# Optimization experiments

Measured on AMD Instinct MI355X. Metric: run time of the kernel, lower is better.

The kernel has to match this reference:

```python
import jax, jax.numpy as jnp
import numpy as np

N = 131072      # points (rays x samples chunk)
E = 8           # spatial sub-networks (centroids)
DIN = 90        # encoded pos+dir features fed to sub-NeRFs (xyz_real=True -> x[:, 3:])
H = 256         # sub-NeRF hidden width
DOUT = 4        # rgb + sigma
MARGIN = 2.0    # boundary_margin
EPS = 1e-8


def setup_inputs() -> dict:
    key = jax.random.key(0)
    k = jax.random.split(key, 5)
    x_xyz = jax.random.uniform(k[0], (N, 3), dtype=jnp.float32)          # routing coords in [0,1)^3
    x_feat = jax.random.normal(k[1], (N, DIN), dtype=jnp.float32)        # encoded features
    x = jnp.concatenate([x_xyz, x_feat], axis=1)                         # [N, 3+DIN]
    centroids = jax.random.uniform(k[2], (E, 3), dtype=jnp.float32)
    W1 = jax.random.normal(k[3], (E, DIN, H), dtype=jnp.float32) * 0.05
    b1 = jnp.zeros((E, H), dtype=jnp.float32)
    W2 = jax.random.normal(k[4], (E, H, DOUT), dtype=jnp.float32) * 0.05
    b2 = jnp.zeros((E, DOUT), dtype=jnp.float32)
    return {"x": x, "centroids": centroids, "W1": W1, "b1": b1, "W2": W2, "b2": b2}


def reference(x, centroids, W1, b1, W2, b2):
    # --- centroid routing (torch.cdist equivalent) ---
    xyz = x[:, :3]                                                       # [N,3]
    d2 = jnp.sum((xyz[:, None, :] - centroids[None, :, :]) ** 2, axis=-1)
    dist = jnp.sqrt(jnp.maximum(d2, 0.0))                                # [N,E]
    inv = 1.0 / (dist + EPS)
    min_d = jnp.min(dist, axis=1, keepdims=True)                         # [N,1]
    inv = jnp.where(dist > MARGIN * min_d, 0.0, inv)                     # zero far experts
    weights = inv / jnp.sum(inv, axis=-1, keepdims=True)                 # [N,E], rows sum to 1

    # --- per-expert sub-NeRF MLP, weighted combine ---
    # Dense-equivalent of masked gather + weighted scatter-add: experts whose
    # weight is exactly 0 contribute nothing, matching the torch masked path.
    feat = x[:, 3:]                                                      # xyz_real=True -> drop xyz
    h = jax.nn.relu(jnp.einsum('nd,edh->enh', feat, W1) + b1[:, None, :])  # [E,N,H]
    out_e = jnp.einsum('enh,eho->eno', h, W2) + b2[:, None, :]             # [E,N,DOUT]
    return jnp.einsum('eno,ne->no', out_e, weights)                        # [N,DOUT]
```

## Files before the change

kernel.cpp:

```cpp
#include <hip/hip_runtime.h>

#define NPTS 131072
#define NE 8
#define DIN 90
#define NH 256

typedef __attribute__((ext_vector_type(8))) short bf16x8;
typedef __attribute__((ext_vector_type(4))) float f32x4;
typedef __attribute__((ext_vector_type(2))) float f32x2;
typedef __attribute__((ext_vector_type(4))) unsigned int u32x4;
typedef __attribute__((ext_vector_type(2))) unsigned int u32x2;
typedef __attribute__((ext_vector_type(4), aligned(4))) float f32x4a;
typedef __attribute__((ext_vector_type(2), aligned(4))) float f32x2a;

__device__ __forceinline__ unsigned short f2bf(float f) {
  unsigned int u = __float_as_uint(f);
  u += 0x7fffu + ((u >> 16) & 1u);
  return (unsigned short)(u >> 16);
}

#if defined(__has_builtin) && __has_builtin(__builtin_amdgcn_cvt_pk_bf16_f32)
typedef __attribute__((ext_vector_type(2))) __bf16 bf16x2;
__device__ __forceinline__ unsigned int pkbf(float f0, float f1) {
  bf16x2 r = __builtin_amdgcn_cvt_pk_bf16_f32(f0, f1);
  return __builtin_bit_cast(unsigned int, r);
}
#else
__device__ __forceinline__ unsigned int pkbf(float f0, float f1) {
  unsigned int u0 = __float_as_uint(f0) + 0x7fffu;
  unsigned int u1 = __float_as_uint(f1) + 0x7fffu;
  return __builtin_amdgcn_perm(u1, u0, 0x07060302u);
}
#endif

__device__ __forceinline__ bf16x8 cvt8(f32x4 a, f32x4 b) {
  u32x4 r;
  r[0] = pkbf(a[0], a[1]);
  r[1] = pkbf(a[2], a[3]);
  r[2] = pkbf(b[0], b[1]);
  r[3] = pkbf(b[2], b[3]);
  return __builtin_bit_cast(bf16x8, r);
}

__global__ __launch_bounds__(256) void prep(const float* __restrict__ W1,
                                            const float* __restrict__ W2,
                                            unsigned short* __restrict__ W1T,
                                            unsigned short* __restrict__ W2T) {
  const int t = threadIdx.x;
  if (blockIdx.x < 32) {
    const int e = blockIdx.x >> 2;
    const int n0 = (blockIdx.x & 3) * 64;
    __shared__ unsigned int ld[64][49];
    const int nl = t & 63;
    const int kq = t >> 6;
#pragma unroll
    for (int j = 0; j < 12; ++j) {
      const int kp2 = kq + 4 * j;
      const int k0 = 2 * kp2, k1 = k0 + 1;
      unsigned int lo = 0, hi = 0;
      if (k0 < DIN) lo = f2bf(W1[((size_t)e * DIN + k0) * NH + n0 + nl]);
      if (k1 < DIN) hi = f2bf(W1[((size_t)e * DIN + k1) * NH + n0 + nl]);
      ld[nl][kp2] = lo | (hi << 16);
    }
    __syncthreads();
    unsigned int* dst = (unsigned int*)(W1T + (size_t)(e * NH + n0) * 96);
#pragma unroll
    for (int j = 0; j < 12; ++j) {
      const int u = t + 256 * j;
      dst[u] = ld[u / 48][u % 48];
    }
  } else {
    __shared__ unsigned short lw[4][264];
    unsigned int* dst = (unsigned int*)W2T;
    for (int e = 0; e < NE; ++e) {
#pragma unroll
      for (int j = 0; j < 4; ++j) {
        const int idx = t + 256 * j;
        lw[idx & 3][idx >> 2] = f2bf(W2[(size_t)e * 1024 + idx]);
      }
      __syncthreads();
#pragma unroll
      for (int j = 0; j < 8; ++j) {
        const int u = t + 256 * j;
        const int o = u >> 7, kp = u & 127;
        unsigned int v = 0;
        if (o < 4)
          v = (unsigned int)lw[o][2 * kp] | ((unsigned int)lw[o][2 * kp + 1] << 16);
        dst[(size_t)e * 2048 + u] = v;
      }
      __syncthreads();
    }
  }
}

__global__ __launch_bounds__(256, 3) void meganerf_main(
    const float* __restrict__ x, const float* __restrict__ cent,
    const float* __restrict__ b1, const float* __restrict__ b2,
    const unsigned short* __restrict__ W1T, const unsigned short* __restrict__ W2T,
    float* __restrict__ out) {
  __shared__ unsigned short sH[4 * 2048];
  __shared__ float sW[NE][64];
  __shared__ float sB2[64][4];
  __shared__ float sB1[NE * NH];

  const int t    = threadIdx.x;
  const int lane = t & 63;
  const int wid  = t >> 6;
  const int l15  = lane & 15;
  const int l4   = lane >> 4;
  const int row0 = blockIdx.x * 64;
  const int gbase = wid * 2048;

#pragma unroll
  for (int j = 0; j < 2; ++j)
    *(f32x4*)&sB1[t * 4 + j * 1024] = *(const f32x4a*)&b1[t * 4 + j * 1024];

#pragma unroll
  for (int j = 0; j < 4; ++j)
    *(u32x4*)&sH[gbase + (j * 64 + lane) * 8] = (u32x4){0u, 0u, 0u, 0u};

  bf16x8 bfr[4][3];
#pragma unroll
  for (int nf = 0; nf < 4; ++nf) {
    const float* gr = x + (size_t)(row0 + 16 * nf + l15) * 93 + 3;
    f32x4 v0, v1;
    v0 = *(const f32x4a*)(gr + 8 * l4);
    v1 = *(const f32x4a*)(gr + 8 * l4 + 4);
    bfr[nf][0] = cvt8(v0, v1);
    v0 = *(const f32x4a*)(gr + 32 + 8 * l4);
    v1 = *(const f32x4a*)(gr + 36 + 8 * l4);
    bfr[nf][1] = cvt8(v0, v1);
    if (l4 < 3) {
      v0 = *(const f32x4a*)(gr + 64 + 8 * l4);
      v1 = *(const f32x4a*)(gr + 68 + 8 * l4);
    } else {
      f32x2 tl = *(const f32x2a*)(gr + 88);
      v0[0] = tl[0]; v0[1] = tl[1]; v0[2] = 0.f; v0[3] = 0.f;
      v1[0] = 0.f; v1[1] = 0.f; v1[2] = 0.f; v1[3] = 0.f;
    }
    bfr[nf][2] = cvt8(v0, v1);
  }

  if (t < 64) {
    const float* gx = x + (size_t)(row0 + t) * 93;
    float px = gx[0], py = gx[1], pz = gx[2];
    float dist[NE], inv[NE];
    float mind = 3.4e38f;
#pragma unroll
    for (int e = 0; e < NE; ++e) {
      float dx = px - cent[e * 3 + 0];
      float dy = py - cent[e * 3 + 1];
      float dz = pz - cent[e * 3 + 2];
      float d2 = dx * dx + dy * dy + dz * dz;
      float d = sqrtf(fmaxf(d2, 0.f));
      dist[e] = d;
      inv[e] = 1.f / (d + 1e-8f);
      mind = fminf(mind, d);
    }
    float s = 0.f;
#pragma unroll
    for (int e = 0; e < NE; ++e) {
      if (dist[e] > 2.0f * mind) inv[e] = 0.f;
      s += inv[e];
    }
    float rs = 1.f / s;
    float bb[4] = {0.f, 0.f, 0.f, 0.f};
#pragma unroll
    for (int e = 0; e < NE; ++e) {
      float w = inv[e] * rs;
      sW[e][t] = w;
#pragma unroll
      for (int o = 0; o < 4; ++o) bb[o] += w * b2[e * 4 + o];
    }
#pragma unroll
    for (int o = 0; o < 4; ++o) sB2[t][o] = bb[o];
  }
  __syncthreads();

  bf16x8 w1buf[2][6];
  bf16x8 bwbuf[2];
  bf16x8 bwprev = __builtin_bit_cast(bf16x8, (u32x4){0u, 0u, 0u, 0u});
  float wv[4];

  auto loadW1 = [&](int idx, int buf) {
    const int e = idx >> 1, c = idx & 1;
    const unsigned short* p =
        W1T + (size_t)(e * NH + 128 * c + 32 * wid + l15) * 96 + 8 * l4;
#pragma unroll
    for (int mf = 0; mf < 2; ++mf)
#pragma unroll
      for (int ks = 0; ks < 3; ++ks)
        w1buf[buf][mf * 3 + ks] = *(const bf16x8*)(p + mf * (16 * 96) + 32 * ks);
  };
  auto loadBW = [&](int idx, int buf) {
    const int e = idx >> 1, c = idx & 1;
    bwbuf[buf] = *(const bf16x8*)(W2T + (size_t)(e * 16 + l15) * NH +
                                  128 * c + 32 * wid + 8 * l4);
  };

  loadBW(0, 0);
  loadW1(0, 0);

  f32x4 facc[4] = {{0.f, 0.f, 0.f, 0.f}, {0.f, 0.f, 0.f, 0.f},
                   {0.f, 0.f, 0.f, 0.f}, {0.f, 0.f, 0.f, 0.f}};

#pragma unroll 2
  for (int i = 0; i < 16; ++i) {
    const int e = i >> 1, c = i & 1, cur = i & 1, nxt = cur ^ 1;
    const int colbase = 128 * c + 32 * wid;

    f32x4 b1v0 = *(const f32x4*)&sB1[e * NH + colbase + 4 * l4];
    f32x4 b1v1 = *(const f32x4*)&sB1[e * NH + colbase + 16 + 4 * l4];

    bf16x8 ah0 = *(const bf16x8*)&sH[gbase + (0 * 64 + lane) * 8];
    bf16x8 ah1 = *(const bf16x8*)&sH[gbase + (1 * 64 + lane) * 8];
    bf16x8 ah2 = *(const bf16x8*)&sH[gbase + (2 * 64 + lane) * 8];
    bf16x8 ah3 = *(const bf16x8*)&sH[gbase + (3 * 64 + lane) * 8];

    if (c == 0) {
#pragma unroll
      for (int nf = 0; nf < 4; ++nf) wv[nf] = sW[e][16 * nf + l15];
    }

    const int ip = (i + 1) & 15;
    loadBW(ip, nxt);
    loadW1(ip, nxt);

#pragma unroll
    for (int mf = 0; mf < 2; ++mf) {
      const f32x4 b1v = (mf == 0) ? b1v0 : b1v1;
      f32x4 acc[4];
#pragma unroll
      for (int nf = 0; nf < 4; ++nf)
        acc[nf] = __builtin_amdgcn_mfma_f32_16x16x32_bf16(
            w1buf[cur][mf * 3 + 0], bfr[nf][0], b1v, 0, 0, 0);
#pragma unroll
      for (int ks = 1; ks < 3; ++ks)
#pragma unroll
        for (int nf = 0; nf < 4; ++nf)
          acc[nf] = __builtin_amdgcn_mfma_f32_16x16x32_bf16(
              w1buf[cur][mf * 3 + ks], bfr[nf][ks], acc[nf], 0, 0, 0);

#pragma unroll
      for (int nf = 0; nf < 4; ++nf) {
        const float w = wv[nf];
        f32x4 a = acc[nf];
        f32x2 p0, p1;
        p0[0] = a[0]; p0[1] = a[1];
        p1[0] = a[2]; p1[1] = a[3];
        const f32x2 z = {0.f, 0.f};
        p0 = __builtin_elementwise_max(p0, z) * w;
        p1 = __builtin_elementwise_max(p1, z) * w;
        u32x2 pk;
        pk[0] = pkbf(p0[0], p0[1]);
        pk[1] = pkbf(p1[0], p1[1]);
        *(u32x2*)&sH[gbase + (nf * 64 + (l15 + 16 * (2 * mf + (l4 >> 1)))) * 8 +
                     4 * (l4 & 1)] = pk;
      }
    }

    facc[0] = __builtin_amdgcn_mfma_f32_16x16x32_bf16(ah0, bwprev, facc[0], 0, 0, 0);
    facc[1] = __builtin_amdgcn_mfma_f32_16x16x32_bf16(ah1, bwprev, facc[1], 0, 0, 0);
    facc[2] = __builtin_amdgcn_mfma_f32_16x16x32_bf16(ah2, bwprev, facc[2], 0, 0, 0);
    facc[3] = __builtin_amdgcn_mfma_f32_16x16x32_bf16(ah3, bwprev, facc[3], 0, 0, 0);

    bwprev = bwbuf[cur];
  }

#pragma unroll
  for (int rf = 0; rf < 4; ++rf) {
    bf16x8 ahf = *(const bf16x8*)&sH[gbase + (rf * 64 + lane) * 8];
    facc[rf] = __builtin_amdgcn_mfma_f32_16x16x32_bf16(ahf, bwprev, facc[rf], 0, 0, 0);
  }

  __syncthreads();
  float* sOutP = (float*)sH;
  if (l15 < 4) {
#pragma unroll
    for (int rf = 0; rf < 4; ++rf)
#pragma unroll
      for (int r = 0; r < 4; ++r)
        sOutP[(wid * 64 + 16 * rf + 4 * l4 + r) * 4 + l15] = facc[rf][r];
  }
  __syncthreads();
  {
    const int row = t >> 2, o = t & 3;
    float v = sB2[row][o] + sOutP[(0 * 64 + row) * 4 + o] + sOutP[(1 * 64 + row) * 4 + o] +
              sOutP[(2 * 64 + row) * 4 + o] + sOutP[(3 * 64 + row) * 4 + o];
    out[row0 * 4 + t] = v;
  }
}

extern "C" void kernel_launch(void* const* d_in, const int* in_sizes, int n_in,
                              void* d_out, int out_size, void* d_ws, size_t ws_size,
                              hipStream_t stream) {
  const float* x    = (const float*)d_in[0];
  const float* cent = (const float*)d_in[1];
  const float* W1   = (const float*)d_in[2];
  const float* b1   = (const float*)d_in[3];
  const float* W2   = (const float*)d_in[4];
  const float* b2   = (const float*)d_in[5];
  float* out = (float*)d_out;

  unsigned short* W1T = (unsigned short*)d_ws;
  unsigned short* W2T = W1T + NE * NH * 96;

  prep<<<33, 256, 0, stream>>>(W1, W2, W1T, W2T);
  meganerf_main<<<NPTS / 64, 256, 0, stream>>>(x, cent, b1, b2, W1T, W2T, out);
}
```

Measured before the change: 174.0 us.

## Feed layer-1 MFMA outputs directly into 16x16x16 MFMAs, drop LDS round-trip

The layer-1 accumulator fragments, after ReLU, scaling and bf16 packing, now serve directly as the A operand of a 16x16x16 bf16 MFMA for the second layer. This removes the shared-memory staging buffer for hidden activations, its zero-init, the per-iteration LDS reads and writes, and the trailing MFMA. W2 is repacked in the prep kernel into a layout matching the register-resident fragments, without LDS or barriers. In exchange, layer 2 issues more, smaller MFMAs per iteration, and there is less overlap between layer-2 work and the next layer-1 chunk.

```diff
diff --git a/kernel.cpp b/kernel.cpp
--- a/kernel.cpp
+++ b/kernel.cpp
@@ -6,6 +6,7 @@
 #define NH 256
 
 typedef __attribute__((ext_vector_type(8))) short bf16x8;
+typedef __attribute__((ext_vector_type(4))) short bf16x4;
 typedef __attribute__((ext_vector_type(4))) float f32x4;
 typedef __attribute__((ext_vector_type(2))) float f32x2;
 typedef __attribute__((ext_vector_type(4))) unsigned int u32x4;
@@ -40,6 +41,16 @@
   r[2] = pkbf(b[0], b[1]);
   r[3] = pkbf(b[2], b[3]);
   return __builtin_bit_cast(bf16x8, r);
+}
+
+__device__ __forceinline__ f32x4 mfma16(bf16x4 a, bf16x4 b, f32x4 c) {
+#if defined(__has_builtin) && __has_builtin(__builtin_amdgcn_mfma_f32_16x16x16bf16_1k)
+  return __builtin_amdgcn_mfma_f32_16x16x16bf16_1k(a, b, c, 0, 0, 0);
+#else
+  f32x4 d = c;
+  asm("v_mfma_f32_16x16x16_bf16 %0, %1, %2, %0" : "+v"(d) : "v"(a), "v"(b));
+  return d;
+#endif
 }
 
 __global__ __launch_bounds__(256) void prep(const float* __restrict__ W1,
@@ -70,25 +81,20 @@
       dst[u] = ld[u / 48][u % 48];
     }
   } else {
-    __shared__ unsigned short lw[4][264];
     unsigned int* dst = (unsigned int*)W2T;
-    for (int e = 0; e < NE; ++e) {
-#pragma unroll
-      for (int j = 0; j < 4; ++j) {
-        const int idx = t + 256 * j;
-        lw[idx & 3][idx >> 2] = f2bf(W2[(size_t)e * 1024 + idx]);
+#pragma unroll 4
+    for (int j = 0; j < 64; ++j) {
+      const int u = t + 256 * j;
+      const int m = u & 7;
+      const int o = (u >> 3) & 15;
+      const int hb = (u >> 7) & 15;
+      const int e = u >> 11;
+      unsigned int lo = 0, hi = 0;
+      if (o < 4) {
+        lo = f2bf(W2[((size_t)e * 256 + hb * 16 + 2 * m) * 4 + o]);
+        hi = f2bf(W2[((size_t)e * 256 + hb * 16 + 2 * m + 1) * 4 + o]);
       }
-      __syncthreads();
-#pragma unroll
-      for (int j = 0; j < 8; ++j) {
-        const int u = t + 256 * j;
-        const int o = u >> 7, kp = u & 127;
-        unsigned int v = 0;
-        if (o < 4)
-          v = (unsigned int)lw[o][2 * kp] | ((unsigned int)lw[o][2 * kp + 1] << 16);
-        dst[(size_t)e * 2048 + u] = v;
-      }
-      __syncthreads();
+      dst[u] = lo | (hi << 16);
     }
   }
 }
@@ -98,7 +104,7 @@
     const float* __restrict__ b1, const float* __restrict__ b2,
     const unsigned short* __restrict__ W1T, const unsigned short* __restrict__ W2T,
     float* __restrict__ out) {
-  __shared__ unsigned short sH[4 * 2048];
+  __shared__ float sOut[4][64][4];
   __shared__ float sW[NE][64];
   __shared__ float sB2[64][4];
   __shared__ float sB1[NE * NH];
@@ -109,15 +115,10 @@
   const int l15  = lane & 15;
   const int l4   = lane >> 4;
   const int row0 = blockIdx.x * 64;
-  const int gbase = wid * 2048;
 
 #pragma unroll
   for (int j = 0; j < 2; ++j)
     *(f32x4*)&sB1[t * 4 + j * 1024] = *(const f32x4a*)&b1[t * 4 + j * 1024];
-
-#pragma unroll
-  for (int j = 0; j < 4; ++j)
-    *(u32x4*)&sH[gbase + (j * 64 + lane) * 8] = (u32x4){0u, 0u, 0u, 0u};
 
   bf16x8 bfr[4][3];
 #pragma unroll
@@ -178,8 +179,7 @@
   __syncthreads();
 
   bf16x8 w1buf[2][6];
-  bf16x8 bwbuf[2];
-  bf16x8 bwprev = __builtin_bit_cast(bf16x8, (u32x4){0u, 0u, 0u, 0u});
+  bf16x4 w2f[2][2];
   float wv[4];
 
   auto loadW1 = [&](int idx, int buf) {
@@ -192,14 +192,16 @@
       for (int ks = 0; ks < 3; ++ks)
         w1buf[buf][mf * 3 + ks] = *(const bf16x8*)(p + mf * (16 * 96) + 32 * ks);
   };
-  auto loadBW = [&](int idx, int buf) {
+  auto loadW2 = [&](int idx, int buf) {
     const int e = idx >> 1, c = idx & 1;
-    bwbuf[buf] = *(const bf16x8*)(W2T + (size_t)(e * 16 + l15) * NH +
-                                  128 * c + 32 * wid + 8 * l4);
+    const int hb0 = 8 * c + 2 * wid;
+    const unsigned short* p = W2T + ((size_t)(e * 16 + hb0) * 256) + l15 * 16 + l4 * 4;
+    w2f[buf][0] = *(const bf16x4*)(p);
+    w2f[buf][1] = *(const bf16x4*)(p + 256);
   };
 
-  loadBW(0, 0);
   loadW1(0, 0);
+  loadW2(0, 0);
 
   f32x4 facc[4] = {{0.f, 0.f, 0.f, 0.f}, {0.f, 0.f, 0.f, 0.f},
                    {0.f, 0.f, 0.f, 0.f}, {0.f, 0.f, 0.f, 0.f}};
@@ -211,20 +213,14 @@
 
     f32x4 b1v0 = *(const f32x4*)&sB1[e * NH + colbase + 4 * l4];
     f32x4 b1v1 = *(const f32x4*)&sB1[e * NH + colbase + 16 + 4 * l4];
-
-    bf16x8 ah0 = *(const bf16x8*)&sH[gbase + (0 * 64 + lane) * 8];
-    bf16x8 ah1 = *(const bf16x8*)&sH[gbase + (1 * 64 + lane) * 8];
-    bf16x8 ah2 = *(const bf16x8*)&sH[gbase + (2 * 64 + lane) * 8];
-    bf16x8 ah3 = *(const bf16x8*)&sH[gbase + (3 * 64 + lane) * 8];
-
     if (c == 0) {
 #pragma unroll
       for (int nf = 0; nf < 4; ++nf) wv[nf] = sW[e][16 * nf + l15];
     }
 
     const int ip = (i + 1) & 15;
-    loadBW(ip, nxt);
     loadW1(ip, nxt);
+    loadW2(ip, nxt);
 
 #pragma unroll
     for (int mf = 0; mf < 2; ++mf) {
@@ -254,39 +250,23 @@
         u32x2 pk;
         pk[0] = pkbf(p0[0], p0[1]);
         pk[1] = pkbf(p1[0], p1[1]);
-        *(u32x2*)&sH[gbase + (nf * 64 + (l15 + 16 * (2 * mf + (l4 >> 1)))) * 8 +
-                     4 * (l4 & 1)] = pk;
+        facc[nf] = mfma16(__builtin_bit_cast(bf16x4, pk), w2f[cur][mf], facc[nf]);
       }
     }
-
-    facc[0] = __builtin_amdgcn_mfma_f32_16x16x32_bf16(ah0, bwprev, facc[0], 0, 0, 0);
-    facc[1] = __builtin_amdgcn_mfma_f32_16x16x32_bf16(ah1, bwprev, facc[1], 0, 0, 0);
-    facc[2] = __builtin_amdgcn_mfma_f32_16x16x32_bf16(ah2, bwprev, facc[2], 0, 0, 0);
-    facc[3] = __builtin_amdgcn_mfma_f32_16x16x32_bf16(ah3, bwprev, facc[3], 0, 0, 0);
-
-    bwprev = bwbuf[cur];
-  }
-
-#pragma unroll
-  for (int rf = 0; rf < 4; ++rf) {
-    bf16x8 ahf = *(const bf16x8*)&sH[gbase + (rf * 64 + lane) * 8];
-    facc[rf] = __builtin_amdgcn_mfma_f32_16x16x32_bf16(ahf, bwprev, facc[rf], 0, 0, 0);
-  }
-
-  __syncthreads();
-  float* sOutP = (float*)sH;
+  }
+
   if (l15 < 4) {
 #pragma unroll
-    for (int rf = 0; rf < 4; ++rf)
+    for (int nf = 0; nf < 4; ++nf)
 #pragma unroll
       for (int r = 0; r < 4; ++r)
-        sOutP[(wid * 64 + 16 * rf + 4 * l4 + r) * 4 + l15] = facc[rf][r];
+        sOut[wid][16 * nf + 4 * l4 + r][l15] = facc[nf][r];
   }
   __syncthreads();
   {
     const int row = t >> 2, o = t & 3;
-    float v = sB2[row][o] + sOutP[(0 * 64 + row) * 4 + o] + sOutP[(1 * 64 + row) * 4 + o] +
-              sOutP[(2 * 64 + row) * 4 + o] + sOutP[(3 * 64 + row) * 4 + o];
+    float v = sB2[row][o] + sOut[0][row][o] + sOut[1][row][o] +
+              sOut[2][row][o] + sOut[3][row][o];
     out[row0 * 4 + t] = v;
   }
 }
```

After: 187.9 us. 8.0% more time.

## Remove deferred second-layer MFMA, parallelize W2 prep, add MFMA priority hints

Applied to the files above, without the earlier changes.

Drops the software-pipelined second-layer MFMA, which read the previous iteration's hidden tile from shared memory, and instead runs it right after writing the current tile. This removes the initial zeroing of sH and the drain loop after the main loop. W2 prep is split across 8 blocks, one per expert, reading global memory directly instead of serializing experts through LDS in a single block. s_setprio hints are added around the MFMA bursts. The trade-off is that each layer-2 read of sH now directly follows the writes to it, which may add a shared-memory dependency stall.

```diff
diff --git a/kernel.cpp b/kernel.cpp
--- a/kernel.cpp
+++ b/kernel.cpp
@@ -70,25 +70,21 @@
       dst[u] = ld[u / 48][u % 48];
     }
   } else {
-    __shared__ unsigned short lw[4][264];
-    unsigned int* dst = (unsigned int*)W2T;
-    for (int e = 0; e < NE; ++e) {
-#pragma unroll
-      for (int j = 0; j < 4; ++j) {
-        const int idx = t + 256 * j;
-        lw[idx & 3][idx >> 2] = f2bf(W2[(size_t)e * 1024 + idx]);
+    const int e = blockIdx.x - 32;
+    unsigned int* dst = (unsigned int*)W2T + (size_t)e * 2048;
+    const float* src = W2 + (size_t)e * 1024;
+#pragma unroll
+    for (int j = 0; j < 8; ++j) {
+      const int u = t + 256 * j;
+      const int o = u >> 7;
+      const int kp = u & 127;
+      unsigned int v = 0;
+      if (o < 4) {
+        unsigned int lo = f2bf(src[(2 * kp) * 4 + o]);
+        unsigned int hi = f2bf(src[(2 * kp + 1) * 4 + o]);
+        v = lo | (hi << 16);
       }
-      __syncthreads();
-#pragma unroll
-      for (int j = 0; j < 8; ++j) {
-        const int u = t + 256 * j;
-        const int o = u >> 7, kp = u & 127;
-        unsigned int v = 0;
-        if (o < 4)
-          v = (unsigned int)lw[o][2 * kp] | ((unsigned int)lw[o][2 * kp + 1] << 16);
-        dst[(size_t)e * 2048 + u] = v;
-      }
-      __syncthreads();
+      dst[u] = v;
     }
   }
 }
@@ -114,10 +110,6 @@
 #pragma unroll
   for (int j = 0; j < 2; ++j)
     *(f32x4*)&sB1[t * 4 + j * 1024] = *(const f32x4a*)&b1[t * 4 + j * 1024];
-
-#pragma unroll
-  for (int j = 0; j < 4; ++j)
-    *(u32x4*)&sH[gbase + (j * 64 + lane) * 8] = (u32x4){0u, 0u, 0u, 0u};
 
   bf16x8 bfr[4][3];
 #pragma unroll
@@ -179,7 +171,6 @@
 
   bf16x8 w1buf[2][6];
   bf16x8 bwbuf[2];
-  bf16x8 bwprev = __builtin_bit_cast(bf16x8, (u32x4){0u, 0u, 0u, 0u});
   float wv[4];
 
   auto loadW1 = [&](int idx, int buf) {
@@ -211,12 +202,6 @@
 
     f32x4 b1v0 = *(const f32x4*)&sB1[e * NH + colbase + 4 * l4];
     f32x4 b1v1 = *(const f32x4*)&sB1[e * NH + colbase + 16 + 4 * l4];
-
-    bf16x8 ah0 = *(const bf16x8*)&sH[gbase + (0 * 64 + lane) * 8];
-    bf16x8 ah1 = *(const bf16x8*)&sH[gbase + (1 * 64 + lane) * 8];
-    bf16x8 ah2 = *(const bf16x8*)&sH[gbase + (2 * 64 + lane) * 8];
-    bf16x8 ah3 = *(const bf16x8*)&sH[gbase + (3 * 64 + lane) * 8];
-
     if (c == 0) {
 #pragma unroll
       for (int nf = 0; nf < 4; ++nf) wv[nf] = sW[e][16 * nf + l15];
@@ -230,6 +215,7 @@
     for (int mf = 0; mf < 2; ++mf) {
       const f32x4 b1v = (mf == 0) ? b1v0 : b1v1;
       f32x4 acc[4];
+      __builtin_amdgcn_s_setprio(1);
 #pragma unroll
       for (int nf = 0; nf < 4; ++nf)
         acc[nf] = __builtin_amdgcn_mfma_f32_16x16x32_bf16(
@@ -240,6 +226,7 @@
         for (int nf = 0; nf < 4; ++nf)
           acc[nf] = __builtin_amdgcn_mfma_f32_16x16x32_bf16(
               w1buf[cur][mf * 3 + ks], bfr[nf][ks], acc[nf], 0, 0, 0);
+      __builtin_amdgcn_s_setprio(0);
 
 #pragma unroll
       for (int nf = 0; nf < 4; ++nf) {
@@ -259,18 +246,13 @@
       }
     }
 
-    facc[0] = __builtin_amdgcn_mfma_f32_16x16x32_bf16(ah0, bwprev, facc[0], 0, 0, 0);
-    facc[1] = __builtin_amdgcn_mfma_f32_16x16x32_bf16(ah1, bwprev, facc[1], 0, 0, 0);
-    facc[2] = __builtin_amdgcn_mfma_f32_16x16x32_bf16(ah2, bwprev, facc[2], 0, 0, 0);
-    facc[3] = __builtin_amdgcn_mfma_f32_16x16x32_bf16(ah3, bwprev, facc[3], 0, 0, 0);
-
-    bwprev = bwbuf[cur];
-  }
-
-#pragma unroll
-  for (int rf = 0; rf < 4; ++rf) {
-    bf16x8 ahf = *(const bf16x8*)&sH[gbase + (rf * 64 + lane) * 8];
-    facc[rf] = __builtin_amdgcn_mfma_f32_16x16x32_bf16(ahf, bwprev, facc[rf], 0, 0, 0);
+    __builtin_amdgcn_s_setprio(1);
+#pragma unroll
+    for (int rf = 0; rf < 4; ++rf) {
+      bf16x8 ah = *(const bf16x8*)&sH[gbase + (rf * 64 + lane) * 8];
+      facc[rf] = __builtin_amdgcn_mfma_f32_16x16x32_bf16(ah, bwbuf[cur], facc[rf], 0, 0, 0);
+    }
+    __builtin_amdgcn_s_setprio(0);
   }
 
   __syncthreads();
@@ -305,6 +287,6 @@
   unsigned short* W1T = (unsigned short*)d_ws;
   unsigned short* W2T = W1T + NE * NH * 96;
 
-  prep<<<33, 256, 0, stream>>>(W1, W2, W1T, W2T);
+  prep<<<40, 256, 0, stream>>>(W1, W2, W1T, W2T);
   meganerf_main<<<NPTS / 64, 256, 0, stream>>>(x, cent, b1, b2, W1T, W2T, out);
 }
```

Result: faster. 163.5 us (median of 2 runs) (-6.0%).
